# Optimization experiments

Measured on AMD Instinct MI355X. Metric: run time of the kernel, lower is better.

## Reference

```python
import jax, jax.numpy as jnp
import numpy as np

N_HEADS = 16


def setup_inputs() -> dict:
    key = jax.random.key(0)
    k1, k2, k3, k4 = jax.random.split(key, 4)
    B, T, C = 2, 2048, 1024
    x = jax.random.normal(k1, (B, T, C), dtype=jnp.float32)
    scale = 1.0 / np.sqrt(C)
    Wq = jax.random.normal(k2, (C, C), dtype=jnp.float32) * scale
    Wk = jax.random.normal(k3, (C, C), dtype=jnp.float32) * scale
    Wv = jax.random.normal(k4, (C, C), dtype=jnp.float32) * scale
    return {"x": x, "Wq": Wq, "Wk": Wk, "Wv": Wv}


def reference(x, Wq, Wk, Wv):
    B, T, C = x.shape
    H = N_HEADS
    Dh = C // H
    # Faithful to original: direct view of (B,T,C) -> (B,H,T,Dh) (no transpose)
    q = (x @ Wq.T).reshape(B, H, T, Dh)
    k = (x @ Wk.T).reshape(B, H, T, Dh)
    v = (x @ Wv.T).reshape(B, H, T, Dh)
    scores = jnp.einsum('bhqd,bhkd->bhqk', q, k) * (1.0 / (Dh ** 0.5))
    mask = jnp.tril(jnp.ones((T, T), dtype=bool))  # causal mask
    scores = jnp.where(mask, scores, -jnp.inf)
    att = jax.nn.softmax(scores, axis=-1)
    out = jnp.einsum('bhqk,bhkd->bhqd', att, v)
    return out.reshape(B, T, C)
```

## Files before the change

### kernel.cpp

```cpp
#include <hip/hip_runtime.h>
#include <hip/hip_bf16.h>
#include <stdint.h>

#define AS1 __attribute__((address_space(1)))
#define AS3 __attribute__((address_space(3)))

typedef __bf16 bf16x8 __attribute__((ext_vector_type(8)));
typedef float  f32x4  __attribute__((ext_vector_type(4)));
typedef unsigned short ushort8v __attribute__((ext_vector_type(8)));
typedef unsigned short ushort4v __attribute__((ext_vector_type(4)));
typedef short short8v __attribute__((ext_vector_type(8)));
typedef short short4v __attribute__((ext_vector_type(4)));

__device__ __forceinline__ unsigned short f2bf(float f) {
    unsigned int u = __float_as_uint(f);
    u += 0x7fffu + ((u >> 16) & 1u);
    return (unsigned short)(u >> 16);
}
__device__ __forceinline__ unsigned int pk2bf(float a, float b) {
    __hip_bfloat162 h = __float22bfloat162_rn(make_float2(a, b));
    unsigned int u;
    __builtin_memcpy(&u, &h, 4);
    return u;
}
__device__ __forceinline__ void g2lds16(const void* gp, void* lp) {
    __builtin_amdgcn_global_load_lds((AS1 void*)gp, (AS3 void*)lp, 16, 0, 0);
}
#define E2(x) __builtin_amdgcn_exp2f(x)

__global__ __launch_bounds__(256) void cast_all(const float* __restrict__ x,
                                                const float* __restrict__ w0,
                                                const float* __restrict__ w1,
                                                const float* __restrict__ w2,
                                                unsigned short* __restrict__ xb,
                                                unsigned short* __restrict__ wc) {
    int id = blockIdx.x;
    const float* s;
    unsigned short* d;
    int base;
    if (id < 4096) { s = x; d = xb; base = id; }
    else {
        int z = (id - 4096) >> 10;
        s = (z == 0) ? w0 : (z == 1) ? w1 : w2;
        d = wc + (size_t)z * 1048576;
        base = (id - 4096) & 1023;
    }
    int i = (base * 256 + threadIdx.x) * 4;
    float4 v = *(const float4*)(s + i);
    ushort4v o = { f2bf(v.x), f2bf(v.y), f2bf(v.z), f2bf(v.w) };
    *(ushort4v*)(d + i) = o;
}

#define VMW(n) asm volatile("s_waitcnt vmcnt(" #n ")" ::: "memory")
#define NOW
#define PH(I, S, CUR, STG, ENDW) do {                                          \
    const int kx_ = ((S) * 32 + quad * 8) ^ ((cl & 4) << 2);                   \
    bf16x8 af_[4], bq_[4];                                                     \
    _Pragma("unroll")                                                          \
    for (int m_ = 0; m_ < 4; ++m_)                                             \
        af_[m_] = *(const bf16x8*)&SA[CUR][((w >> 2) * 128 + ((I) * 4 + m_) * 16 + cl) * 64 + kx_]; \
    _Pragma("unroll")                                                          \
    for (int n_ = 0; n_ < 4; ++n_)                                             \
        bq_[n_] = *(const bf16x8*)&SB[CUR][((w & 3) * 64 + n_ * 16 + cl) * 64 + kx_]; \
    STG;                                                                       \
    __builtin_amdgcn_s_barrier();                                              \
    asm volatile("s_waitcnt lgkmcnt(0)" ::: "memory");                         \
    __builtin_amdgcn_sched_barrier(0);                                         \
    __builtin_amdgcn_s_setprio(1);                                             \
    _Pragma("unroll")                                                          \
    for (int m_ = 0; m_ < 4; ++m_)                                             \
        _Pragma("unroll")                                                      \
        for (int n_ = 0; n_ < 4; ++n_)                                         \
            acc[(I) * 4 + m_][n_] = __builtin_amdgcn_mfma_f32_16x16x32_bf16(   \
                af_[m_], bq_[n_], acc[(I) * 4 + m_][n_], 0, 0, 0);             \
    __builtin_amdgcn_s_setprio(0);                                             \
    __builtin_amdgcn_sched_barrier(0);                                         \
    ENDW;                                                                      \
    __builtin_amdgcn_s_barrier();                                              \
} while (0)

__global__ __launch_bounds__(512, 2) void gemm_qkv(const unsigned short* __restrict__ X,
                                                   const unsigned short* __restrict__ W,
                                                   unsigned short* __restrict__ QKV) {
    const int K = 1024, N = 1024;
    const int b = blockIdx.x;
    const int z = b >> 6;
    const int r = b & 63;
    const int m0 = (r >> 2) * 256;
    const int n0 = (r & 3) * 256;

    const unsigned short* A = X;
    const unsigned short* Bp = W + (size_t)z * (1024 * 1024);
    unsigned short* C = QKV + (size_t)z * (4096 * 1024);
    const float qs = (z == 0) ? 0.18033688011112042f : 1.0f;

    __shared__ unsigned short SA[2][16384];
    __shared__ unsigned short SB[2][16384];

    const int t = threadIdx.x;
    const int w = t >> 6;
    const int l = t & 63;
    const int cl = l & 15;
    const int quad = l >> 4;

    const int srow8 = t >> 3;
    const int klog = ((t & 7) * 8) ^ (((t >> 5) & 1) << 4);
    const unsigned short* Abase = A + (size_t)(m0 + srow8) * K + klog;
    const unsigned short* Bbase = Bp + (size_t)(n0 + srow8) * K + klog;
    unsigned short* const sa0 = &SA[0][w * 512];
    unsigned short* const sa1 = &SA[1][w * 512];
    unsigned short* const sb0 = &SB[0][w * 512];
    unsigned short* const sb1 = &SB[1][w * 512];

    f32x4 acc[8][4] = {};

#define STGA(nb, q, k0) g2lds16(Abase + (size_t)(q) * 65536 + (k0), ((nb) ? sa1 : sa0) + (q) * 4096)
#define STGB(nb, q, k0) g2lds16(Bbase + (size_t)(q) * 65536 + (k0), ((nb) ? sb1 : sb0) + (q) * 4096)

    STGB(0, 0, 0); STGB(0, 1, 0); STGB(0, 2, 0); STGB(0, 3, 0);
    STGA(0, 0, 0); STGA(0, 2, 0); STGA(0, 1, 0); STGA(0, 3, 0);
    VMW(2);
    __builtin_amdgcn_s_barrier();

    for (int tt = 0; tt < 15; ++tt) {
        const int cur = tt & 1, nxt = cur ^ 1;
        const int k1 = (tt + 1) * 64;
        PH(0, 0, cur, { STGB(nxt, 0, k1); STGB(nxt, 1, k1); }, NOW);
        PH(0, 1, cur, { STGB(nxt, 2, k1); STGB(nxt, 3, k1); }, VMW(4));
        PH(1, 0, cur, { STGA(nxt, 0, k1); STGA(nxt, 2, k1); }, NOW);
        PH(1, 1, cur, { STGA(nxt, 1, k1); STGA(nxt, 3, k1); }, VMW(2));
    }
    PH(0, 0, 1, {}, NOW);
    PH(0, 1, 1, {}, VMW(0));
    PH(1, 0, 1, {}, NOW);
    PH(1, 1, 1, {}, NOW);

#undef STGA
#undef STGB

    #pragma unroll
    for (int mf = 0; mf < 8; ++mf) {
        #pragma unroll
        for (int rr = 0; rr < 4; ++rr) {
            size_t row = (size_t)(m0 + (w >> 2) * 128 + mf * 16 + quad * 4 + rr);
            #pragma unroll
            for (int nf = 0; nf < 4; ++nf)
                C[row * N + (n0 + (w & 3) * 64 + nf * 16 + cl)] = f2bf(acc[mf][nf][rr] * qs);
        }
    }
}

__global__ __launch_bounds__(256) void vtrans(const unsigned short* __restrict__ Vn,
                                              unsigned short* __restrict__ V3) {
    const int bh = blockIdx.y;
    const int T0 = blockIdx.x * 128;
    __shared__ unsigned short L[128 * 72];
    const int t = threadIdx.x;

    const unsigned short* src = Vn + (size_t)bh * 131072 + (size_t)T0 * 64;
    #pragma unroll
    for (int p = 0; p < 4; ++p) {
        int r = p * 32 + (t >> 3), c = (t & 7) * 8;
        *(ushort8v*)(L + r * 72 + c) = *(const ushort8v*)(src + (size_t)r * 64 + c);
    }
    __syncthreads();
    unsigned short* dst = V3 + (size_t)bh * 131072 + (size_t)(T0 >> 4) * 1024;
    #pragma unroll
    for (int p = 0; p < 2; ++p) {
        int item = p * 256 + t;
        int kb = item >> 6, cl = (item >> 2) & 15, qk = item & 3;
        ushort8v a, b;
        #pragma unroll
        for (int u = 0; u < 8; ++u) {
            int dt = u >> 2, j = u & 3;
            a[u] = L[(kb * 16 + qk * 4 + j) * 72 + dt * 16 + cl];
            b[u] = L[(kb * 16 + qk * 4 + j) * 72 + (dt + 2) * 16 + cl];
        }
        unsigned short* dp = dst + kb * 1024 + cl * 64 + qk * 16;
        *(ushort8v*)(dp) = a;
        *(ushort8v*)(dp + 8) = b;
    }
}

__global__ __launch_bounds__(256, 4) void attn(const unsigned short* __restrict__ QK,
                                               const unsigned short* __restrict__ V3,
                                               float* __restrict__ Out) {
    const int id = blockIdx.x;
    const int bh = id & 31;
    const int bb = 31 - (id >> 5);
    const int t = threadIdx.x;
    const int w = t >> 6;
    const int l = t & 63;
    const int cl = l & 15;
    const int quad = l >> 4;
    const int c7 = cl & 7;

    const size_t bhoff = (size_t)bh * 131072;
    const unsigned short* Qb = QK + bhoff;
    const unsigned short* Kb = QK + (size_t)4194304 + bhoff;
    const unsigned short* Vb = V3 + bhoff;
    float* Ob = Out + bhoff;

    __shared__ unsigned short KVs[2][8192];

    const int g2 = t + 256;
    const int kO1 = (t >> 3) * 64 + (((t & 7) ^ ((t >> 3) & 7)) * 8);
    const int kO2 = (g2 >> 3) * 64 + (((g2 & 7) ^ ((g2 >> 3) & 7)) * 8);
    const int wg1 = t & 63;
    const int wg2 = g2 & 63;
    const int vO1 = (t >> 6) * 512 + ((wg1 ^ ((wg1 >> 3) & 7)) * 8);
    const int vO2 = (g2 >> 6) * 512 + ((wg2 ^ ((wg2 >> 3) & 7)) * 8);
    const int lB1 = w * 512;
    const int lB2 = 2048 + w * 512;

    const int oK0 = cl * 64 + (((quad)     ^ c7) * 8);
    const int oK1 = cl * 64 + (((quad + 4) ^ c7) * 8);
    const int oV0 = cl * 64 + (((quad * 2)     ^ c7) * 8);
    const int oV1 = cl * 64 + (((quad * 2 + 1) ^ c7) * 8);

    const int mrel = w * 16 + cl;
    const int nch = bb + 1;
    const int m0w = bb * 64 + w * 16;

    bf16x8 qf0, qf1;
    {
        const unsigned short* qa = Qb + (size_t)(m0w + cl) * 64 + quad * 8;
        qf0 = *(const bf16x8*)(qa);
        qf1 = *(const bf16x8*)(qa + 32);
    }

    f32x4 o[4] = {};
    float lps = 0.f;

    {
        unsigned short* s = &KVs[0][0];
        g2lds16(Kb + kO1, s + lB1);
        g2lds16(Kb + kO2, s + lB2);
        g2lds16(Vb + vO1, s + 4096 + lB1);
        g2lds16(Vb + vO2, s + 4096 + lB2);
    }

    for (int c = 0; c < nch; ++c) {
        __syncthreads();
        if (c + 1 < nch) {
            unsigned short* s = &KVs[(c + 1) & 1][0];
            const size_t off = (size_t)(c + 1) * 4096;
            g2lds16(Kb + off + kO1, s + lB1);
            g2lds16(Kb + off + kO2, s + lB2);
            g2lds16(Vb + off + vO1, s + 4096 + lB1);
            g2lds16(Vb + off + vO2, s + 4096 + lB2);
        }
        const unsigned short* Kl = &KVs[c & 1][0];
        const unsigned short* Vl = Kl + 4096;
        const bool masked = (c == bb);

        bf16x8 kf0[4], kf1[4];
        #pragma unroll
        for (int kt = 0; kt < 4; ++kt) {
            kf0[kt] = *(const bf16x8*)(Kl + kt * 1024 + oK0);
            kf1[kt] = *(const bf16x8*)(Kl + kt * 1024 + oK1);
        }
        f32x4 st[4] = {};
        __builtin_amdgcn_s_setprio(1);
        #pragma unroll
        for (int kt = 0; kt < 4; ++kt) {
            st[kt] = __builtin_amdgcn_mfma_f32_16x16x32_bf16(kf0[kt], qf0, st[kt], 0, 0, 0);
            st[kt] = __builtin_amdgcn_mfma_f32_16x16x32_bf16(kf1[kt], qf1, st[kt], 0, 0, 0);
        }
        __builtin_amdgcn_s_setprio(0);

        short4v pb[4];
        #pragma unroll
        for (int kt = 0; kt < 4; ++kt) {
            float p0, p1, p2, p3;
            if (masked) {
                const int lk = kt * 16 + quad * 4;
                p0 = (lk     <= mrel) ? E2(st[kt][0]) : 0.f;
                p1 = (lk + 1 <= mrel) ? E2(st[kt][1]) : 0.f;
                p2 = (lk + 2 <= mrel) ? E2(st[kt][2]) : 0.f;
                p3 = (lk + 3 <= mrel) ? E2(st[kt][3]) : 0.f;
            } else {
                p0 = E2(st[kt][0]);
                p1 = E2(st[kt][1]);
                p2 = E2(st[kt][2]);
                p3 = E2(st[kt][3]);
            }
            lps += (p0 + p1) + (p2 + p3);
            uint2 u = { pk2bf(p0, p1), pk2bf(p2, p3) };
            short4v pv;
            __builtin_memcpy(&pv, &u, 8);
            pb[kt] = pv;
        }

        __builtin_amdgcn_s_setprio(1);
        #pragma unroll
        for (int kt = 0; kt < 4; ++kt) {
            short8v v0 = *(const short8v*)(Vl + kt * 1024 + oV0);
            short8v v1 = *(const short8v*)(Vl + kt * 1024 + oV1);
            short4v a0 = __builtin_shufflevector(v0, v0, 0, 1, 2, 3);
            short4v a1 = __builtin_shufflevector(v0, v0, 4, 5, 6, 7);
            short4v a2 = __builtin_shufflevector(v1, v1, 0, 1, 2, 3);
            short4v a3 = __builtin_shufflevector(v1, v1, 4, 5, 6, 7);
            o[0] = __builtin_amdgcn_mfma_f32_16x16x16bf16_1k(a0, pb[kt], o[0], 0, 0, 0);
            o[1] = __builtin_amdgcn_mfma_f32_16x16x16bf16_1k(a1, pb[kt], o[1], 0, 0, 0);
            o[2] = __builtin_amdgcn_mfma_f32_16x16x16bf16_1k(a2, pb[kt], o[2], 0, 0, 0);
            o[3] = __builtin_amdgcn_mfma_f32_16x16x16bf16_1k(a3, pb[kt], o[3], 0, 0, 0);
        }
        __builtin_amdgcn_s_setprio(0);
    }

    lps += __shfl_xor(lps, 16);
    lps += __shfl_xor(lps, 32);
    const float inv = 1.0f / lps;
    #pragma unroll
    for (int dt = 0; dt < 4; ++dt) {
        f32x4 r = o[dt];
        r[0] *= inv; r[1] *= inv; r[2] *= inv; r[3] *= inv;
        *(f32x4*)(Ob + (size_t)(m0w + cl) * 64 + dt * 16 + quad * 4) = r;
    }
}

extern "C" void kernel_launch(void* const* d_in, const int* in_sizes, int n_in,
                              void* d_out, int out_size, void* d_ws, size_t ws_size,
                              hipStream_t stream) {
    const float* x  = (const float*)d_in[0];
    const float* Wq = (const float*)d_in[1];
    const float* Wk = (const float*)d_in[2];
    const float* Wv = (const float*)d_in[3];
    float* out = (float*)d_out;

    unsigned short* xb  = (unsigned short*)d_ws;
    unsigned short* wc  = xb + (size_t)4096 * 1024;
    unsigned short* qkv = wc + (size_t)3 * 1024 * 1024;
    unsigned short* vt  = qkv + (size_t)3 * 4096 * 1024;

    hipLaunchKernelGGL(cast_all, dim3(7168), dim3(256), 0, stream, x, Wq, Wk, Wv, xb, wc);
    hipLaunchKernelGGL(gemm_qkv, dim3(192), dim3(512), 0, stream, xb, wc, qkv);
    hipLaunchKernelGGL(vtrans, dim3(16, 32), dim3(256), 0, stream, qkv + (size_t)2 * 4096 * 1024, vt);
    hipLaunchKernelGGL(attn, dim3(1024), dim3(256), 0, stream, qkv, vt, out);
}
```

Before: 150.3 us.

## Reorder QKV GEMM phases to reuse B fragments and widen LDS swizzle

Changes the QKV projection GEMM's phase order so each k-half runs both M halves back to back. The B-operand fragments loaded in the first phase are kept in registers and reused in the second, which removes half of the LDS reads for B. It also changes the LDS XOR swizzle from a single-bit pattern to a full 3-bit row-based pattern to cut bank conflicts, and moves the vmcnt waits to match the new staging order. The risks are higher register pressure from holding bqr, and possible hazards if the new wait placement lets a buffer be read before its staged loads have landed.

```diff
diff --git a/kernel.cpp b/kernel.cpp
--- a/kernel.cpp
+++ b/kernel.cpp
@@ -53,30 +53,52 @@
 
 #define VMW(n) asm volatile("s_waitcnt vmcnt(" #n ")" ::: "memory")
 #define NOW
-#define PH(I, S, CUR, STG, ENDW) do {                                          \
-    const int kx_ = ((S) * 32 + quad * 8) ^ ((cl & 4) << 2);                   \
-    bf16x8 af_[4], bq_[4];                                                     \
-    _Pragma("unroll")                                                          \
-    for (int m_ = 0; m_ < 4; ++m_)                                             \
-        af_[m_] = *(const bf16x8*)&SA[CUR][((w >> 2) * 128 + ((I) * 4 + m_) * 16 + cl) * 64 + kx_]; \
-    _Pragma("unroll")                                                          \
-    for (int n_ = 0; n_ < 4; ++n_)                                             \
-        bq_[n_] = *(const bf16x8*)&SB[CUR][((w & 3) * 64 + n_ * 16 + cl) * 64 + kx_]; \
+#define PHCORE(STG, MFMAS, ENDW) do {                                          \
     STG;                                                                       \
     __builtin_amdgcn_s_barrier();                                              \
     asm volatile("s_waitcnt lgkmcnt(0)" ::: "memory");                         \
     __builtin_amdgcn_sched_barrier(0);                                         \
     __builtin_amdgcn_s_setprio(1);                                             \
-    _Pragma("unroll")                                                          \
-    for (int m_ = 0; m_ < 4; ++m_)                                             \
-        _Pragma("unroll")                                                      \
-        for (int n_ = 0; n_ < 4; ++n_)                                         \
-            acc[(I) * 4 + m_][n_] = __builtin_amdgcn_mfma_f32_16x16x32_bf16(   \
-                af_[m_], bq_[n_], acc[(I) * 4 + m_][n_], 0, 0, 0);             \
+    MFMAS;                                                                     \
     __builtin_amdgcn_s_setprio(0);                                             \
     __builtin_amdgcn_sched_barrier(0);                                         \
     ENDW;                                                                      \
     __builtin_amdgcn_s_barrier();                                              \
+} while (0)
+
+#define PHA(S, CUR, STG, ENDW) do {                                            \
+    const int kx_ = ((S) * 32 + quad * 8) ^ ((cl & 7) * 8);                    \
+    bf16x8 af_[4];                                                             \
+    _Pragma("unroll")                                                          \
+    for (int m_ = 0; m_ < 4; ++m_)                                             \
+        af_[m_] = *(const bf16x8*)&SA[CUR][(rowA0 + m_ * 16) * 64 + kx_];      \
+    _Pragma("unroll")                                                          \
+    for (int n_ = 0; n_ < 4; ++n_)                                             \
+        bqr[n_] = *(const bf16x8*)&SB[CUR][(rowB0 + n_ * 16) * 64 + kx_];      \
+    PHCORE(STG,                                                                \
+        _Pragma("unroll")                                                      \
+        for (int m_ = 0; m_ < 4; ++m_)                                         \
+            _Pragma("unroll")                                                  \
+            for (int n_ = 0; n_ < 4; ++n_)                                     \
+                acc[m_][n_] = __builtin_amdgcn_mfma_f32_16x16x32_bf16(         \
+                    af_[m_], bqr[n_], acc[m_][n_], 0, 0, 0);                   \
+        , ENDW);                                                               \
+} while (0)
+
+#define PHB(S, CUR, STG, ENDW) do {                                            \
+    const int kx_ = ((S) * 32 + quad * 8) ^ ((cl & 7) * 8);                    \
+    bf16x8 af_[4];                                                             \
+    _Pragma("unroll")                                                          \
+    for (int m_ = 0; m_ < 4; ++m_)                                             \
+        af_[m_] = *(const bf16x8*)&SA[CUR][(rowA0 + 64 + m_ * 16) * 64 + kx_]; \
+    PHCORE(STG,                                                                \
+        _Pragma("unroll")                                                      \
+        for (int m_ = 0; m_ < 4; ++m_)                                         \
+            _Pragma("unroll")                                                  \
+            for (int n_ = 0; n_ < 4; ++n_)                                     \
+                acc[4 + m_][n_] = __builtin_amdgcn_mfma_f32_16x16x32_bf16(     \
+                    af_[m_], bqr[n_], acc[4 + m_][n_], 0, 0, 0);               \
+        , ENDW);                                                               \
 } while (0)
 
 __global__ __launch_bounds__(512, 2) void gemm_qkv(const unsigned short* __restrict__ X,
@@ -102,9 +124,11 @@
     const int l = t & 63;
     const int cl = l & 15;
     const int quad = l >> 4;
+    const int rowA0 = (w >> 2) * 128 + cl;
+    const int rowB0 = (w & 3) * 64 + cl;
 
     const int srow8 = t >> 3;
-    const int klog = ((t & 7) * 8) ^ (((t >> 5) & 1) << 4);
+    const int klog = (((t & 7) ^ ((t >> 3) & 7)) * 8);
     const unsigned short* Abase = A + (size_t)(m0 + srow8) * K + klog;
     const unsigned short* Bbase = Bp + (size_t)(n0 + srow8) * K + klog;
     unsigned short* const sa0 = &SA[0][w * 512];
@@ -113,6 +137,7 @@
     unsigned short* const sb1 = &SB[1][w * 512];
 
     f32x4 acc[8][4] = {};
+    bf16x8 bqr[4];
 
 #define STGA(nb, q, k0) g2lds16(Abase + (size_t)(q) * 65536 + (k0), ((nb) ? sa1 : sa0) + (q) * 4096)
 #define STGB(nb, q, k0) g2lds16(Bbase + (size_t)(q) * 65536 + (k0), ((nb) ? sb1 : sb0) + (q) * 4096)
@@ -125,15 +150,15 @@
     for (int tt = 0; tt < 15; ++tt) {
         const int cur = tt & 1, nxt = cur ^ 1;
         const int k1 = (tt + 1) * 64;
-        PH(0, 0, cur, { STGB(nxt, 0, k1); STGB(nxt, 1, k1); }, NOW);
-        PH(0, 1, cur, { STGB(nxt, 2, k1); STGB(nxt, 3, k1); }, VMW(4));
-        PH(1, 0, cur, { STGA(nxt, 0, k1); STGA(nxt, 2, k1); }, NOW);
-        PH(1, 1, cur, { STGA(nxt, 1, k1); STGA(nxt, 3, k1); }, VMW(2));
-    }
-    PH(0, 0, 1, {}, NOW);
-    PH(0, 1, 1, {}, VMW(0));
-    PH(1, 0, 1, {}, NOW);
-    PH(1, 1, 1, {}, NOW);
+        PHA(0, cur, { STGB(nxt, 0, k1); STGB(nxt, 1, k1); }, VMW(2));
+        PHB(0, cur, { STGB(nxt, 2, k1); STGB(nxt, 3, k1); }, NOW);
+        PHA(1, cur, { STGA(nxt, 0, k1); STGA(nxt, 2, k1); }, NOW);
+        PHB(1, cur, { STGA(nxt, 1, k1); STGA(nxt, 3, k1); }, VMW(2));
+    }
+    PHA(0, 1, {}, VMW(0));
+    PHB(0, 1, {}, NOW);
+    PHA(1, 1, {}, NOW);
+    PHB(1, 1, {}, NOW);
 
 #undef STGA
 #undef STGB
```

After: 145.8 us. 1.03x faster.
